# Performance work log

Hardware: AMD Instinct MI355X
Metric: run time of the kernel (lower is better)

## Reference

```python
import jax, jax.numpy as jnp
import numpy as np

UP = 2  # scale factor

def make_kernel(vals, factor):
    k = jnp.asarray(vals, dtype=jnp.float32)
    k = k[None, :] * k[:, None]          # 1D -> separable 2D
    k = k / k.sum()
    return k * (factor ** 2)             # gain for upsampling

def setup_inputs() -> dict:
    key = jax.random.key(0)
    x = jax.random.normal(key, (8, 128, 128, 128), dtype=jnp.float32)
    kernel = make_kernel([1.0, 3.0, 3.0, 1.0], UP)  # (4,4)
    return {"inp_tensor": x, "kernel": kernel}

def reference(inp_tensor, kernel):
    # upfirdn2d(x, k, up=2, down=1, pad=(pad0, pad1)) fused via dilated conv:
    # lhs_dilation performs the zero-insertion upsample without materializing
    # the big zero tensor; extra (UP-1) right/bottom pad matches StyleGAN2's
    # trailing zeros after zero-insertion.
    kh, kw = kernel.shape
    p = kh - UP
    pad0 = (p + 1) // 2 + UP - 1
    pad1 = p // 2
    n, c, h, w = inp_tensor.shape
    x = inp_tensor.reshape(n * c, 1, h, w)
    # torch impl does F.conv2d with flipped kernel == true convolution with k;
    # lax conv is correlation, so flip to match (k is symmetric here anyway).
    wk = jnp.flip(kernel, (0, 1))[None, None]  # (1,1,kh,kw)
    out = jax.lax.conv_general_dilated(
        x, wk,
        window_strides=(1, 1),
        padding=((pad0, pad1 + UP - 1), (pad0, pad1 + UP - 1)),
        lhs_dilation=(UP, UP),
        dimension_numbers=("NCHW", "OIHW", "NCHW"),
    )
    return out.reshape(n, c, h * UP, w * UP)
```

## Files before the change

### kernel.cpp

```cpp
#include <hip/hip_runtime.h>

#define NC   1024
#define H    128
#define W    128
#define OH   256
#define OW   256

__global__ __launch_bounds__(256) void upscale_kernel(
    const float* __restrict__ x,
    const float* __restrict__ K,
    float* __restrict__ out)
{
    int gid = blockIdx.x * blockDim.x + threadIdx.x;
    int ot = gid & 63;
    int oy = (gid >> 6) & 255;
    int nc = gid >> 14;

    int iy = oy >> 1;
    int ay = oy & 1;
    int j0 = ot << 1;

    int r0  = iy;
    int r1  = ay ? iy + 1 : iy - 1;
    int sy0 = ay ? 2 : 1;
    int sy1 = ay ? 0 : 3;
    bool r1ok = (unsigned)r1 < (unsigned)H;

    const float* base = x + (size_t)nc * (H * W);

    float a0, a1, a2, a3;
    {
        const float* p = base + r0 * W + j0;
        a1 = p[0];
        a2 = p[1];
        a0 = (j0 > 0)     ? p[-1] : 0.f;
        a3 = (j0 + 2 < W) ? p[2]  : 0.f;
    }
    float b0 = 0.f, b1 = 0.f, b2 = 0.f, b3 = 0.f;
    if (r1ok) {
        const float* p = base + r1 * W + j0;
        b1 = p[0];
        b2 = p[1];
        b0 = (j0 > 0)     ? p[-1] : 0.f;
        b3 = (j0 + 2 < W) ? p[2]  : 0.f;
    }

    float k00 = K[sy0 * 4 + 0], k01 = K[sy0 * 4 + 1],
          k02 = K[sy0 * 4 + 2], k03 = K[sy0 * 4 + 3];
    float k10 = K[sy1 * 4 + 0], k11 = K[sy1 * 4 + 1],
          k12 = K[sy1 * 4 + 2], k13 = K[sy1 * 4 + 3];

    float4 o4;
    o4.x = k01 * a1 + k03 * a0 + k11 * b1 + k13 * b0;
    o4.y = k00 * a2 + k02 * a1 + k10 * b2 + k12 * b1;
    o4.z = k01 * a2 + k03 * a1 + k11 * b2 + k13 * b1;
    o4.w = k00 * a3 + k02 * a2 + k10 * b3 + k12 * b2;

    float4* po = (float4*)(out + (size_t)nc * (OH * OW) + (size_t)oy * OW + (ot << 2));
    *po = o4;
}

extern "C" void kernel_launch(void* const* d_in, const int* in_sizes, int n_in,
                              void* d_out, int out_size, void* d_ws, size_t ws_size,
                              hipStream_t stream) {
    const float* x   = (const float*)d_in[0];
    const float* K   = (const float*)d_in[1];
    float*       out = (float*)d_out;

    const int total_threads = NC * OH * (OW / 4);
    dim3 block(256);
    dim3 grid(total_threads / 256);
    upscale_kernel<<<grid, block, 0, stream>>>(x, K, out);
}
```

Baseline: 369.1 us.

## Compute 2x8 output tile per thread with float4 loads and shuffles

```diff
diff --git a/kernel.cpp b/kernel.cpp
--- a/kernel.cpp
+++ b/kernel.cpp
@@ -6,58 +6,63 @@
 #define OH   256
 #define OW   256
 
+
+__device__ __forceinline__ void accum(float L, const float4& v, float R,
+                                      const float4& kr, float o[8]) {
+    float e1 = kr.y, e3 = kr.w;
+    float c0 = kr.x, c2 = kr.z;
+    o[0] += e1 * v.x + e3 * L;
+    o[1] += c0 * v.y + c2 * v.x;
+    o[2] += e1 * v.y + e3 * v.x;
+    o[3] += c0 * v.z + c2 * v.y;
+    o[4] += e1 * v.z + e3 * v.y;
+    o[5] += c0 * v.w + c2 * v.z;
+    o[6] += e1 * v.w + e3 * v.z;
+    o[7] += c0 * R   + c2 * v.w;
+}
+
 __global__ __launch_bounds__(256) void upscale_kernel(
     const float* __restrict__ x,
-    const float* __restrict__ K,
+    const float* __restrict__ Kp,
     float* __restrict__ out)
 {
     int gid = blockIdx.x * blockDim.x + threadIdx.x;
-    int ot = gid & 63;
-    int oy = (gid >> 6) & 255;
-    int nc = gid >> 14;
+    int jg = gid & 31;
+    int iy = (gid >> 5) & (H - 1);
+    int nc = gid >> 12;
 
-    int iy = oy >> 1;
-    int ay = oy & 1;
-    int j0 = ot << 1;
+    const float4* row = (const float4*)(x + (size_t)nc * (H * W));
+    const float4 z = make_float4(0.f, 0.f, 0.f, 0.f);
 
-    int r0  = iy;
-    int r1  = ay ? iy + 1 : iy - 1;
-    int sy0 = ay ? 2 : 1;
-    int sy1 = ay ? 0 : 3;
-    bool r1ok = (unsigned)r1 < (unsigned)H;
+    float4 vm = (iy > 0)     ? row[(size_t)(iy - 1) * (W / 4) + jg] : z;
+    float4 v0 =                row[(size_t)iy       * (W / 4) + jg];
+    float4 vp = (iy < H - 1) ? row[(size_t)(iy + 1) * (W / 4) + jg] : z;
 
-    const float* base = x + (size_t)nc * (H * W);
+    float Lm = __shfl_up(vm.w, 1, 32);
+    float L0 = __shfl_up(v0.w, 1, 32);
+    float Lp = __shfl_up(vp.w, 1, 32);
+    float Rm = __shfl_down(vm.x, 1, 32);
+    float R0 = __shfl_down(v0.x, 1, 32);
+    float Rp = __shfl_down(vp.x, 1, 32);
+    if (jg == 0)     { Lm = 0.f; L0 = 0.f; Lp = 0.f; }
+    if (jg == W/4-1) { Rm = 0.f; R0 = 0.f; Rp = 0.f; }
 
-    float a0, a1, a2, a3;
-    {
-        const float* p = base + r0 * W + j0;
-        a1 = p[0];
-        a2 = p[1];
-        a0 = (j0 > 0)     ? p[-1] : 0.f;
-        a3 = (j0 + 2 < W) ? p[2]  : 0.f;
-    }
-    float b0 = 0.f, b1 = 0.f, b2 = 0.f, b3 = 0.f;
-    if (r1ok) {
-        const float* p = base + r1 * W + j0;
-        b1 = p[0];
-        b2 = p[1];
-        b0 = (j0 > 0)     ? p[-1] : 0.f;
-        b3 = (j0 + 2 < W) ? p[2]  : 0.f;
-    }
+    const float4* K4 = (const float4*)Kp;
+    float4 k0 = K4[0], k1 = K4[1], k2 = K4[2], k3 = K4[3];
 
-    float k00 = K[sy0 * 4 + 0], k01 = K[sy0 * 4 + 1],
-          k02 = K[sy0 * 4 + 2], k03 = K[sy0 * 4 + 3];
-    float k10 = K[sy1 * 4 + 0], k11 = K[sy1 * 4 + 1],
-          k12 = K[sy1 * 4 + 2], k13 = K[sy1 * 4 + 3];
+    float oe[8] = {0.f, 0.f, 0.f, 0.f, 0.f, 0.f, 0.f, 0.f};
+    accum(L0, v0, R0, k1, oe);
+    accum(Lm, vm, Rm, k3, oe);
+    float oo[8] = {0.f, 0.f, 0.f, 0.f, 0.f, 0.f, 0.f, 0.f};
+    accum(L0, v0, R0, k2, oo);
+    accum(Lp, vp, Rp, k0, oo);
 
-    float4 o4;
-    o4.x = k01 * a1 + k03 * a0 + k11 * b1 + k13 * b0;
-    o4.y = k00 * a2 + k02 * a1 + k10 * b2 + k12 * b1;
-    o4.z = k01 * a2 + k03 * a1 + k11 * b2 + k13 * b1;
-    o4.w = k00 * a3 + k02 * a2 + k10 * b3 + k12 * b2;
-
-    float4* po = (float4*)(out + (size_t)nc * (OH * OW) + (size_t)oy * OW + (ot << 2));
-    *po = o4;
+    float* ob = out + (size_t)nc * (OH * OW) + (size_t)(2 * iy) * OW + 8 * jg;
+    ((float4*)ob)[0] = make_float4(oe[0], oe[1], oe[2], oe[3]);
+    ((float4*)ob)[1] = make_float4(oe[4], oe[5], oe[6], oe[7]);
+    float* ob2 = ob + OW;
+    ((float4*)ob2)[0] = make_float4(oo[0], oo[1], oo[2], oo[3]);
+    ((float4*)ob2)[1] = make_float4(oo[4], oo[5], oo[6], oo[7]);
 }
 
 extern "C" void kernel_launch(void* const* d_in, const int* in_sizes, int n_in,
@@ -67,7 +72,7 @@
     const float* K   = (const float*)d_in[1];
     float*       out = (float*)d_out;
 
-    const int total_threads = NC * OH * (OW / 4);
+    const int total_threads = NC * H * (W / 4);
     dim3 block(256);
     dim3 grid(total_threads / 256);
     upscale_kernel<<<grid, block, 0, stream>>>(x, K, out);
```

After: 336.7 us. 1.1x faster.
